# Performance work log

Measured on AMD Instinct MI355X. Metric: run time of the kernel, lower is better.

## Reference

```python
import jax, jax.numpy as jnp
import numpy as np

K = 2           # top-k experts
TEMP = 1.0      # router temperature


def setup_inputs() -> dict:
    key = jax.random.key(0)
    k0, k1, k2, k3 = jax.random.split(key, 4)
    B, T, C, E = 4, 8192, 1024, 64
    x = jax.random.normal(k0, (B, T, C), dtype=jnp.float32)
    cond = jax.random.normal(k1, (B, C), dtype=jnp.float32)
    # nn.Linear weights: gate (E, C), cond_proj (C, 2C)
    Wg = jax.random.normal(k2, (E, C), dtype=jnp.float32) * 0.02
    Wc = jax.random.normal(k3, (C, 2 * C), dtype=jnp.float32) * 0.02
    return {"x": x, "cond": cond, "Wg": Wg, "Wc": Wc}


def reference(x, cond, Wg, Wc):
    B, T, C = x.shape
    E = Wg.shape[0]
    # conditioning path: broadcast cond over tokens, concat, project
    c_exp = jnp.broadcast_to(cond[:, None, :], (B, T, C))
    hc = jnp.concatenate([x, c_exp], axis=-1)          # (B,T,2C)
    h = jnp.einsum('btd,cd->btc', hc, Wc)              # (B,T,C)
    logits = jnp.einsum('btc,ec->bte', h, Wg) * (1.0 / TEMP)  # (B,T,E)
    probs = jax.nn.softmax(logits, axis=-1)
    topk_vals, idx = jax.lax.top_k(logits, K)          # (B,T,K), sorted desc
    scores = jax.nn.softmax(topk_vals, axis=-1)
    # aux stats (no_grad in torch)
    importance = jax.lax.stop_gradient(jnp.mean(probs, axis=(0, 1)))  # (E,)
    counts = jnp.zeros((E,), probs.dtype).at[idx.reshape(-1)].add(1.0)
    load = counts / jnp.clip(jnp.sum(counts), 1.0)
    load = jax.lax.stop_gradient(load)
    return (idx, scores, probs, importance, load)
```

## Files before the change

### kernel.cpp

```cpp
#include <hip/hip_runtime.h>
#include <math.h>

#define B_    4
#define T_    8192
#define C_    1024
#define E_    64
#define NTOK  (B_*T_)
#define KSEL  2

#define OFF_IDX    0
#define OFF_SCORES (NTOK*KSEL)
#define OFF_PROBS  (2*NTOK*KSEL)
#define OFF_IMP    (OFF_PROBS + NTOK*E_)
#define OFF_LOAD   (OFF_IMP + E_)

#define WS_W32    0
#define WS_BSWH   262144
#define WS_BSWL   393216
#define WS_LB64   524288
#define WS_CNT    526336
#define WS_LIST   526400

#define REFINE_CAP 8192
#define REFINE_EPS 3e-4f

typedef __attribute__((ext_vector_type(8))) short short8;
typedef __attribute__((ext_vector_type(4))) float f32x4;

__global__ __launch_bounds__(256) void k_prep(const float* __restrict__ Wg,
                                              const float* __restrict__ Wc,
                                              const float* __restrict__ cond,
                                              float* __restrict__ wcomb32,
                                              short* __restrict__ bswH,
                                              short* __restrict__ bswL,
                                              double* __restrict__ lbias64,
                                              float* __restrict__ out) {
    __shared__ float wg_s[64 * 64];
    __shared__ float wc_s[64 * 8];
    __shared__ double red[256];

    const int tid = threadIdx.x;
    const int e   = tid & 63;
    const int dg  = tid >> 6;
    const int d0  = blockIdx.x * 8;

    if (blockIdx.x == 0 && tid < 2 * E_) out[OFF_IMP + tid] = 0.f;

    double acc0 = 0.0, acc1 = 0.0;

    for (int c0 = 0; c0 < C_; c0 += 64) {
        __syncthreads();
#pragma unroll
        for (int k = 0; k < 4; ++k) {
            int li = tid + k * 256;
            int r = li >> 4, c4 = (li & 15) * 4;
            float4 v = *(const float4*)&Wg[(size_t)r * 1024 + c0 + c4];
            wg_s[(c4 + 0) * 64 + r] = v.x;
            wg_s[(c4 + 1) * 64 + r] = v.y;
            wg_s[(c4 + 2) * 64 + r] = v.z;
            wg_s[(c4 + 3) * 64 + r] = v.w;
        }
        {
            int cc = tid >> 2, dd0 = (tid & 3) * 2;
            *(float2*)&wc_s[cc * 8 + dd0] =
                *(const float2*)&Wc[(size_t)(c0 + cc) * 2048 + d0 + dd0];
        }
        __syncthreads();
#pragma unroll 4
        for (int c = 0; c < 64; ++c) {
            double wg = (double)wg_s[c * 64 + e];
            acc0 += wg * (double)wc_s[c * 8 + dg * 2 + 0];
            acc1 += wg * (double)wc_s[c * 8 + dg * 2 + 1];
        }
    }

    if (d0 < 1024) {
        double av[2] = {acc0, acc1};
        const int et = e >> 4, nn = e & 15;
#pragma unroll
        for (int j2 = 0; j2 < 2; ++j2) {
            int d = d0 + dg * 2 + j2;
            float f = (float)av[j2];
            wcomb32[d * 64 + e] = f;
            unsigned u = __float_as_uint(f);
            short hi = (short)(u >> 16);
            float r = f - __uint_as_float(u & 0xFFFF0000u);
            short lo = (short)(__float_as_uint(r) >> 16);
            int kchunk = d >> 5, qsel = (d >> 3) & 3, j = d & 7;
            int idx = ((kchunk * 4 + et) * 64 + qsel * 16 + nn) * 8 + j;
            bswH[idx] = hi;
            bswL[idx] = lo;
        }
    } else {
        const int da = d0 - 1024 + dg * 2;
#pragma unroll
        for (int b = 0; b < 4; ++b) {
            double pb = (double)cond[b * 1024 + da] * acc0 +
                        (double)cond[b * 1024 + da + 1] * acc1;
            __syncthreads();
            red[tid] = pb;
            __syncthreads();
            if (tid < 64) {
                double s = red[tid] + red[tid + 64] + red[tid + 128] + red[tid + 192];
#if __has_builtin(__builtin_amdgcn_global_atomic_fadd_f64)
                unsafeAtomicAdd(&lbias64[b * 64 + tid], s);
#else
                atomicAdd(&lbias64[b * 64 + tid], s);
#endif
            }
        }
    }
}

__device__ __forceinline__ void split8(const float* xv, short8& h, short8& l) {
#pragma unroll
    for (int j = 0; j < 8; ++j) {
        unsigned u = __float_as_uint(xv[j]);
        h[j] = (short)(u >> 16);
        float r = xv[j] - __uint_as_float(u & 0xFFFF0000u);
        l[j] = (short)(__float_as_uint(r) >> 16);
    }
}

#define MT    64
#define XSTR  132
#define ROWP  65

__global__ __launch_bounds__(256, 2) void k_main(const float* __restrict__ x,
                                                 const short* __restrict__ bswH,
                                                 const short* __restrict__ bswL,
                                                 const double* __restrict__ lbias64,
                                                 float* __restrict__ out,
                                                 unsigned int* __restrict__ ref_cnt,
                                                 int* __restrict__ ref_list) {
    __shared__ float xs[MT * XSTR];
    __shared__ float invs[MT];
    __shared__ unsigned int cnts[E_];

    const int tid    = threadIdx.x;
    const int wid    = tid >> 6;
    const int lane   = tid & 63;
    const int nn     = lane & 15;
    const int qsel   = lane >> 4;
    const int token0 = blockIdx.x * MT;
    const int b      = token0 >> 13;

    if (tid < E_) cnts[tid] = 0;

    f32x4 acc[4];
#pragma unroll
    for (int et = 0; et < 4; ++et) acc[et] = (f32x4){0.f, 0.f, 0.f, 0.f};

    const int srow = tid >> 5;
    const int scol = (tid & 31) * 4;

    for (int t = 0; t < 8; ++t) {
        const int k0 = t * 128;
#pragma unroll
        for (int p = 0; p < 8; ++p) {
            int row = p * 8 + srow;
            f32x4 v = __builtin_nontemporal_load(
                (const f32x4*)&x[(size_t)(token0 + row) * 1024 + k0 + scol]);
            *(f32x4*)&xs[row * XSTR + scol] = v;
        }
        __syncthreads();
        const float* arow = &xs[(wid * 16 + nn) * XSTR + qsel * 8];
#pragma unroll
        for (int kc = 0; kc < 4; ++kc) {
            float xv[8];
            *(f32x4*)&xv[0] = *(const f32x4*)(arow + kc * 32);
            *(f32x4*)&xv[4] = *(const f32x4*)(arow + kc * 32 + 4);
            short8 ah, al;
            split8(xv, ah, al);
            const int kchunk = t * 4 + kc;
            const short* bh = bswH + (size_t)(kchunk * 4) * 512 + lane * 8;
            const short* bl = bswL + (size_t)(kchunk * 4) * 512 + lane * 8;
#pragma unroll
            for (int et = 0; et < 4; ++et) {
                short8 b_h = *(const short8*)(bh + et * 512);
                short8 b_l = *(const short8*)(bl + et * 512);
                acc[et] = __builtin_amdgcn_mfma_f32_16x16x32_bf16(ah, b_h, acc[et], 0, 0, 0);
                acc[et] = __builtin_amdgcn_mfma_f32_16x16x32_bf16(ah, b_l, acc[et], 0, 0, 0);
                acc[et] = __builtin_amdgcn_mfma_f32_16x16x32_bf16(al, b_h, acc[et], 0, 0, 0);
            }
        }
        __syncthreads();
    }

    const int q4 = qsel * 4;
#pragma unroll
    for (int et = 0; et < 4; ++et) {
        float lb = (float)lbias64[b * 64 + et * 16 + nn];
#pragma unroll
        for (int r = 0; r < 4; ++r) {
            int tok = wid * 16 + q4 + r;
            xs[tok * ROWP + et * 16 + nn] = acc[et][r] + lb;
        }
    }
    __syncthreads();

    if (tid < MT) {
        const int t = tid;
        const int base = t * ROWP;
        float v1 = -1e30f, v2 = -1e30f, v3 = -1e30f;
        int i1 = 0, i2 = 0;
        for (int e = 0; e < E_; ++e) {
            float l = xs[base + e];
            if (l > v1)      { v3 = v2; v2 = v1; i2 = i1; v1 = l; i1 = e; }
            else if (l > v2) { v3 = v2; v2 = l; i2 = e; }
            else if (l > v3) { v3 = l; }
        }
        float sum = 0.f;
        for (int e = 0; e < E_; ++e) {
            float ex = __expf(xs[base + e] - v1);
            xs[base + e] = ex;
            sum += ex;
        }
        invs[t] = 1.0f / sum;

        const int gt = token0 + t;
        float s1 = 1.0f / (1.0f + __expf(v2 - v1));
        *(float2*)&out[OFF_IDX + (size_t)gt * 2]    = make_float2((float)i1, (float)i2);
        *(float2*)&out[OFF_SCORES + (size_t)gt * 2] = make_float2(s1, 1.0f - s1);
        atomicAdd(&cnts[i1], 1u);
        atomicAdd(&cnts[i2], 1u);

        float g12 = v1 - v2, g23 = v2 - v3;
        float g = g12 < g23 ? g12 : g23;
        if (g < REFINE_EPS) {
            unsigned int pos = atomicAdd(ref_cnt, 1u);
            if (pos < REFINE_CAP) ref_list[pos] = gt;
        }
    }
    __syncthreads();

    float* probs = out + OFF_PROBS + (size_t)token0 * E_;
#pragma unroll
    for (int k = 0; k < 4; ++k) {
        int li4 = tid + k * 256;
        int tok = li4 >> 4;
        int c4 = (li4 & 15) << 2;
        float inv = invs[tok];
        int o = tok * ROWP + c4;
        *(float4*)&probs[(size_t)li4 * 4] =
            make_float4(xs[o] * inv, xs[o + 1] * inv,
                        xs[o + 2] * inv, xs[o + 3] * inv);
    }

    if (tid < E_) {
        const int e = tid;
        float s = 0.f;
        for (int t = 0; t < MT; ++t) s += xs[t * ROWP + e] * invs[t];
        atomicAdd(&out[OFF_IMP + e],  s * (1.0f / (float)NTOK));
        atomicAdd(&out[OFF_LOAD + e], (float)cnts[e] * (1.0f / (float)(NTOK * KSEL)));
    }
}

__global__ __launch_bounds__(256) void k_refine(const float* __restrict__ x,
                                                const float* __restrict__ wcomb32,
                                                const double* __restrict__ lbias64,
                                                const unsigned int* __restrict__ ref_cnt,
                                                const int* __restrict__ ref_list,
                                                float* __restrict__ out) {
    int wave = (int)((blockIdx.x * blockDim.x + threadIdx.x) >> 6);
    int lane = threadIdx.x & 63;
    unsigned int n = *ref_cnt;
    if (n > REFINE_CAP) n = REFINE_CAP;
    const int nwaves = (int)((gridDim.x * blockDim.x) >> 6);

    for (unsigned int wi = wave; wi < n; wi += nwaves) {
        const int gt = ref_list[wi];
        const int b = gt / T_;
        const float* xrow = x + (size_t)gt * C_;
        double a0 = 0.0, a1 = 0.0, a2 = 0.0, a3 = 0.0;
        for (int d = 0; d < C_; d += 4) {
            a0 += (double)xrow[d + 0] * (double)wcomb32[(d + 0) * 64 + lane];
            a1 += (double)xrow[d + 1] * (double)wcomb32[(d + 1) * 64 + lane];
            a2 += (double)xrow[d + 2] * (double)wcomb32[(d + 2) * 64 + lane];
            a3 += (double)xrow[d + 3] * (double)wcomb32[(d + 3) * 64 + lane];
        }
        double acc = ((a0 + a1) + (a2 + a3)) + lbias64[b * 64 + lane];

        double v = acc; int id = lane;
        for (int off = 32; off > 0; off >>= 1) {
            double ov = __shfl_xor(v, off, 64);
            int oid   = __shfl_xor(id, off, 64);
            if (ov > v || (ov == v && oid < id)) { v = ov; id = oid; }
        }
        double v1 = v; int i1 = id;
        v = (lane == i1) ? -1e300 : acc; id = lane;
        for (int off = 32; off > 0; off >>= 1) {
            double ov = __shfl_xor(v, off, 64);
            int oid   = __shfl_xor(id, off, 64);
            if (ov > v || (ov == v && oid < id)) { v = ov; id = oid; }
        }
        double v2 = v; int i2 = id;

        if (lane == 0) {
            float s1 = (float)(1.0 / (1.0 + exp(v2 - v1)));
            *(float2*)&out[OFF_IDX + (size_t)gt * 2]    = make_float2((float)i1, (float)i2);
            *(float2*)&out[OFF_SCORES + (size_t)gt * 2] = make_float2(s1, 1.0f - s1);
        }
    }
}

extern "C" void kernel_launch(void* const* d_in, const int* in_sizes, int n_in,
                              void* d_out, int out_size, void* d_ws, size_t ws_size,
                              hipStream_t stream) {
    const float* x    = (const float*)d_in[0];
    const float* cond = (const float*)d_in[1];
    const float* Wg   = (const float*)d_in[2];
    const float* Wc   = (const float*)d_in[3];
    float* out = (float*)d_out;
    char*  ws  = (char*)d_ws;

    float*  wcomb32 = (float*)(ws + WS_W32);
    short*  bswH    = (short*)(ws + WS_BSWH);
    short*  bswL    = (short*)(ws + WS_BSWL);
    double* lbias64 = (double*)(ws + WS_LB64);
    unsigned int* ref_cnt = (unsigned int*)(ws + WS_CNT);
    int*    ref_list = (int*)(ws + WS_LIST);

    hipMemsetAsync(ws + WS_LB64, 0, (WS_CNT - WS_LB64) + 64, stream);

    k_prep<<<256, 256, 0, stream>>>(Wg, Wc, cond, wcomb32, bswH, bswL, lbias64, out);
    k_main<<<NTOK / MT, 256, 0, stream>>>(x, bswH, bswL, lbias64, out, ref_cnt, ref_list);
    k_refine<<<128, 256, 0, stream>>>(x, wcomb32, lbias64, ref_cnt, ref_list, out);
}
```

Measured before the change: 350.9 us.

## Double-buffer x tiles in main kernel with smaller token tiles and split expert work

The main GEMM kernel now uses 32-token tiles held in double-buffered shared memory, and the next k-slice is prefetched into registers while MFMAs run on the current one. Each wave now covers half the tokens and half the expert tiles, and the occupancy hint rises to 4 blocks per SM. This is meant to hide global-load latency and raise parallelism. The prep kernel is also split to 4 output columns per block with twice as many blocks, and the refine grid is doubled. In exchange, B fragments are reloaded across waves and the nontemporal load hint is dropped.

Result: faster. 342.2 us (-2.5%).

```diff
diff --git a/kernel.cpp b/kernel.cpp
--- a/kernel.cpp
+++ b/kernel.cpp
@@ -36,17 +36,17 @@
                                               double* __restrict__ lbias64,
                                               float* __restrict__ out) {
     __shared__ float wg_s[64 * 64];
-    __shared__ float wc_s[64 * 8];
+    __shared__ float wc_s[64 * 4];
     __shared__ double red[256];
 
     const int tid = threadIdx.x;
     const int e   = tid & 63;
     const int dg  = tid >> 6;
-    const int d0  = blockIdx.x * 8;
+    const int d0  = blockIdx.x * 4;
 
     if (blockIdx.x == 0 && tid < 2 * E_) out[OFF_IMP + tid] = 0.f;
 
-    double acc0 = 0.0, acc1 = 0.0;
+    double ae = 0.0, ao = 0.0;
 
     for (int c0 = 0; c0 < C_; c0 += 64) {
         __syncthreads();
@@ -60,43 +60,38 @@
             wg_s[(c4 + 2) * 64 + r] = v.z;
             wg_s[(c4 + 3) * 64 + r] = v.w;
         }
-        {
-            int cc = tid >> 2, dd0 = (tid & 3) * 2;
-            *(float2*)&wc_s[cc * 8 + dd0] =
+        if (tid < 128) {
+            int cc = tid >> 1, dd0 = (tid & 1) * 2;
+            *(float2*)&wc_s[cc * 4 + dd0] =
                 *(const float2*)&Wc[(size_t)(c0 + cc) * 2048 + d0 + dd0];
         }
         __syncthreads();
-#pragma unroll 4
-        for (int c = 0; c < 64; ++c) {
-            double wg = (double)wg_s[c * 64 + e];
-            acc0 += wg * (double)wc_s[c * 8 + dg * 2 + 0];
-            acc1 += wg * (double)wc_s[c * 8 + dg * 2 + 1];
-        }
-    }
+#pragma unroll 8
+        for (int c = 0; c < 64; c += 2) {
+            ae += (double)wg_s[(c + 0) * 64 + e] * (double)wc_s[(c + 0) * 4 + dg];
+            ao += (double)wg_s[(c + 1) * 64 + e] * (double)wc_s[(c + 1) * 4 + dg];
+        }
+    }
+    const double acc = ae + ao;
 
     if (d0 < 1024) {
-        double av[2] = {acc0, acc1};
+        const int d = d0 + dg;
         const int et = e >> 4, nn = e & 15;
-#pragma unroll
-        for (int j2 = 0; j2 < 2; ++j2) {
-            int d = d0 + dg * 2 + j2;
-            float f = (float)av[j2];
-            wcomb32[d * 64 + e] = f;
-            unsigned u = __float_as_uint(f);
-            short hi = (short)(u >> 16);
-            float r = f - __uint_as_float(u & 0xFFFF0000u);
-            short lo = (short)(__float_as_uint(r) >> 16);
-            int kchunk = d >> 5, qsel = (d >> 3) & 3, j = d & 7;
-            int idx = ((kchunk * 4 + et) * 64 + qsel * 16 + nn) * 8 + j;
-            bswH[idx] = hi;
-            bswL[idx] = lo;
-        }
+        float f = (float)acc;
+        wcomb32[d * 64 + e] = f;
+        unsigned u = __float_as_uint(f);
+        short hi = (short)(u >> 16);
+        float r = f - __uint_as_float(u & 0xFFFF0000u);
+        short lo = (short)(__float_as_uint(r) >> 16);
+        int kchunk = d >> 5, qsel = (d >> 3) & 3, j = d & 7;
+        int idx = ((kchunk * 4 + et) * 64 + qsel * 16 + nn) * 8 + j;
+        bswH[idx] = hi;
+        bswL[idx] = lo;
     } else {
-        const int da = d0 - 1024 + dg * 2;
+        const int da = d0 - 1024 + dg;
 #pragma unroll
         for (int b = 0; b < 4; ++b) {
-            double pb = (double)cond[b * 1024 + da] * acc0 +
-                        (double)cond[b * 1024 + da + 1] * acc1;
+            double pb = (double)cond[b * 1024 + da] * acc;
             __syncthreads();
             red[tid] = pb;
             __syncthreads();
@@ -122,18 +117,19 @@
     }
 }
 
-#define MT    64
+#define MT    32
 #define XSTR  132
+#define BUFSZ (MT * XSTR)
 #define ROWP  65
 
-__global__ __launch_bounds__(256, 2) void k_main(const float* __restrict__ x,
+__global__ __launch_bounds__(256, 4) void k_main(const float* __restrict__ x,
                                                  const short* __restrict__ bswH,
                                                  const short* __restrict__ bswL,
                                                  const double* __restrict__ lbias64,
                                                  float* __restrict__ out,
                                                  unsigned int* __restrict__ ref_cnt,
                                                  int* __restrict__ ref_list) {
-    __shared__ float xs[MT * XSTR];
+    __shared__ float xs[2 * BUFSZ];
     __shared__ float invs[MT];
     __shared__ unsigned int cnts[E_];
 
@@ -142,29 +138,41 @@
     const int lane   = tid & 63;
     const int nn     = lane & 15;
     const int qsel   = lane >> 4;
+    const int th     = wid & 1;
+    const int eh     = wid >> 1;
+    const int et0    = eh * 2;
     const int token0 = blockIdx.x * MT;
     const int b      = token0 >> 13;
 
     if (tid < E_) cnts[tid] = 0;
 
-    f32x4 acc[4];
-#pragma unroll
-    for (int et = 0; et < 4; ++et) acc[et] = (f32x4){0.f, 0.f, 0.f, 0.f};
+    f32x4 acc[2];
+#pragma unroll
+    for (int ei = 0; ei < 2; ++ei) acc[ei] = (f32x4){0.f, 0.f, 0.f, 0.f};
 
     const int srow = tid >> 5;
     const int scol = (tid & 31) * 4;
 
+    f32x4 rg[4];
+#pragma unroll
+    for (int p = 0; p < 4; ++p)
+        rg[p] = *(const f32x4*)&x[(size_t)(token0 + p * 8 + srow) * 1024 + scol];
+#pragma unroll
+    for (int p = 0; p < 4; ++p)
+        *(f32x4*)&xs[(p * 8 + srow) * XSTR + scol] = rg[p];
+    __syncthreads();
+
+    const float* arow0 = &xs[(th * 16 + nn) * XSTR + qsel * 8];
+
     for (int t = 0; t < 8; ++t) {
-        const int k0 = t * 128;
-#pragma unroll
-        for (int p = 0; p < 8; ++p) {
-            int row = p * 8 + srow;
-            f32x4 v = __builtin_nontemporal_load(
-                (const f32x4*)&x[(size_t)(token0 + row) * 1024 + k0 + scol]);
-            *(f32x4*)&xs[row * XSTR + scol] = v;
-        }
-        __syncthreads();
-        const float* arow = &xs[(wid * 16 + nn) * XSTR + qsel * 8];
+        const int cur = t & 1;
+        if (t < 7) {
+            const int k0 = (t + 1) * 128;
+#pragma unroll
+            for (int p = 0; p < 4; ++p)
+                rg[p] = *(const f32x4*)&x[(size_t)(token0 + p * 8 + srow) * 1024 + k0 + scol];
+        }
+        const float* arow = arow0 + cur * BUFSZ;
 #pragma unroll
         for (int kc = 0; kc < 4; ++kc) {
             float xv[8];
@@ -173,35 +181,41 @@
             short8 ah, al;
             split8(xv, ah, al);
             const int kchunk = t * 4 + kc;
-            const short* bh = bswH + (size_t)(kchunk * 4) * 512 + lane * 8;
-            const short* bl = bswL + (size_t)(kchunk * 4) * 512 + lane * 8;
-#pragma unroll
-            for (int et = 0; et < 4; ++et) {
-                short8 b_h = *(const short8*)(bh + et * 512);
-                short8 b_l = *(const short8*)(bl + et * 512);
-                acc[et] = __builtin_amdgcn_mfma_f32_16x16x32_bf16(ah, b_h, acc[et], 0, 0, 0);
-                acc[et] = __builtin_amdgcn_mfma_f32_16x16x32_bf16(ah, b_l, acc[et], 0, 0, 0);
-                acc[et] = __builtin_amdgcn_mfma_f32_16x16x32_bf16(al, b_h, acc[et], 0, 0, 0);
+            const short* bh = bswH + (size_t)(kchunk * 4 + et0) * 512 + lane * 8;
+            const short* bl = bswL + (size_t)(kchunk * 4 + et0) * 512 + lane * 8;
+#pragma unroll
+            for (int ei = 0; ei < 2; ++ei) {
+                short8 b_h = *(const short8*)(bh + ei * 512);
+                short8 b_l = *(const short8*)(bl + ei * 512);
+                acc[ei] = __builtin_amdgcn_mfma_f32_16x16x32_bf16(ah, b_h, acc[ei], 0, 0, 0);
+                acc[ei] = __builtin_amdgcn_mfma_f32_16x16x32_bf16(ah, b_l, acc[ei], 0, 0, 0);
+                acc[ei] = __builtin_amdgcn_mfma_f32_16x16x32_bf16(al, b_h, acc[ei], 0, 0, 0);
             }
         }
+        if (t < 7) {
+#pragma unroll
+            for (int p = 0; p < 4; ++p)
+                *(f32x4*)&xs[(cur ^ 1) * BUFSZ + (p * 8 + srow) * XSTR + scol] = rg[p];
+        }
         __syncthreads();
     }
 
     const int q4 = qsel * 4;
 #pragma unroll
-    for (int et = 0; et < 4; ++et) {
+    for (int ei = 0; ei < 2; ++ei) {
+        const int et = et0 + ei;
         float lb = (float)lbias64[b * 64 + et * 16 + nn];
 #pragma unroll
         for (int r = 0; r < 4; ++r) {
-            int tok = wid * 16 + q4 + r;
-            xs[tok * ROWP + et * 16 + nn] = acc[et][r] + lb;
+            int tok = th * 16 + q4 + r;
+            xs[tok * ROWP + et * 16 + nn] = acc[ei][r] + lb;
         }
     }
     __syncthreads();
 
     if (tid < MT) {
-        const int t = tid;
-        const int base = t * ROWP;
+        const int tk = tid;
+        const int base = tk * ROWP;
         float v1 = -1e30f, v2 = -1e30f, v3 = -1e30f;
         int i1 = 0, i2 = 0;
         for (int e = 0; e < E_; ++e) {
@@ -216,9 +230,9 @@
             xs[base + e] = ex;
             sum += ex;
         }
-        invs[t] = 1.0f / sum;
-
-        const int gt = token0 + t;
+        invs[tk] = 1.0f / sum;
+
+        const int gt = token0 + tk;
         float s1 = 1.0f / (1.0f + __expf(v2 - v1));
         *(float2*)&out[OFF_IDX + (size_t)gt * 2]    = make_float2((float)i1, (float)i2);
         *(float2*)&out[OFF_SCORES + (size_t)gt * 2] = make_float2(s1, 1.0f - s1);
@@ -236,7 +250,7 @@
 
     float* probs = out + OFF_PROBS + (size_t)token0 * E_;
 #pragma unroll
-    for (int k = 0; k < 4; ++k) {
+    for (int k = 0; k < 2; ++k) {
         int li4 = tid + k * 256;
         int tok = li4 >> 4;
         int c4 = (li4 & 15) << 2;
@@ -250,7 +264,7 @@
     if (tid < E_) {
         const int e = tid;
         float s = 0.f;
-        for (int t = 0; t < MT; ++t) s += xs[t * ROWP + e] * invs[t];
+        for (int tt = 0; tt < MT; ++tt) s += xs[tt * ROWP + e] * invs[tt];
         atomicAdd(&out[OFF_IMP + e],  s * (1.0f / (float)NTOK));
         atomicAdd(&out[OFF_LOAD + e], (float)cnts[e] * (1.0f / (float)(NTOK * KSEL)));
     }
@@ -323,7 +337,7 @@
 
     hipMemsetAsync(ws + WS_LB64, 0, (WS_CNT - WS_LB64) + 64, stream);
 
-    k_prep<<<256, 256, 0, stream>>>(Wg, Wc, cond, wcomb32, bswH, bswL, lbias64, out);
+    k_prep<<<512, 256, 0, stream>>>(Wg, Wc, cond, wcomb32, bswH, bswL, lbias64, out);
     k_main<<<NTOK / MT, 256, 0, stream>>>(x, bswH, bswL, lbias64, out, ref_cnt, ref_list);
-    k_refine<<<128, 256, 0, stream>>>(x, wcomb32, lbias64, ref_cnt, ref_list, out);
-}
+    k_refine<<<256, 256, 0, stream>>>(x, wcomb32, lbias64, ref_cnt, ref_list, out);
+}
```
